# Kernel tuning notes

Hardware: AMD Instinct MI355X
Metric: run time of the kernel (lower is better)

Reference implementation:

```python
import jax, jax.numpy as jnp
import numpy as np

E = 160000      # num edges
N = 10000       # num nodes
M1 = 16         # rep1.mult
M2 = 8          # rep2.mult (output)
D1 = 3          # rep1.dim
D2 = 3          # rep2.dim
NREPS = 2       # repr.nreps()
EDGE_DIM = 32
HID = 64
NHEADS = 4
HIDDEN_SIZE = M2 * D2            # 24, attention hidden size
HEAD_DIM = HIDDEN_SIZE // NHEADS # 6
M2H = 3 * M2                     # repr_h.rep2.mult = 24 (k,q,v fused)
TMP_OUT = NREPS * M1 * M2H       # 768, RadialWeight layer2 out dim


def setup_inputs() -> dict:
    key = jax.random.key(0)
    ks = jax.random.split(key, 9)
    src = jax.random.randint(ks[0], (E,), 0, N)
    dst = jax.random.randint(ks[1], (E,), 0, N)
    basis = jax.random.normal(ks[2], (E, D1, NREPS * D2), dtype=jnp.float32)
    edge_feats = jax.random.normal(ks[3], (E, EDGE_DIM), dtype=jnp.float32)
    f = jax.random.normal(ks[4], (N, M1, D1), dtype=jnp.float32)
    W1 = jax.random.normal(ks[5], (HID, EDGE_DIM), dtype=jnp.float32) * 0.05
    b1 = jnp.zeros((HID,), dtype=jnp.float32)
    W2 = jax.random.normal(ks[6], (TMP_OUT, HID), dtype=jnp.float32) * 0.05
    b2 = jnp.zeros((TMP_OUT,), dtype=jnp.float32)
    return {"src": src, "dst": dst, "basis": basis, "edge_feats": edge_feats,
            "f": f, "W1": W1, "b1": b1, "W2": W2, "b2": b2}


def reference(src, dst, basis, edge_feats, f, W1, b1, W2, b2):
    # --- RadialWeight: 2-layer MLP on invariant edge feats ---
    h = jax.nn.relu(edge_feats @ W1.T + b1)               # (E, HID)
    rw = (h @ W2.T + b2).reshape(E, M2H, M1 * NREPS)      # (E, 3*m2, m1*nreps)

    # --- Equivariant convolution: gather by src, basis matmul, radial mix ---
    fe = f[src]                                           # (E, m1, d1)
    tmp = jnp.einsum('emd,edk->emk', fe, basis)           # (E, m1, nreps*d2)
    tmp = tmp.reshape(E, M1 * NREPS, D2)                  # (E, m1*nreps, d2)
    conv = jnp.einsum('ecm,emd->ecd', rw, tmp)            # (E, 3*m2, d2)

    # --- split into k, q, v along the multiplicity (feature) dim ---
    k, q, v = jnp.split(conv, 3, axis=1)                  # each (E, m2, d2)
    k = k.reshape(E, NHEADS, HEAD_DIM)
    q = q.reshape(E, NHEADS, HEAD_DIM)
    v = v.reshape(E, NHEADS, HEAD_DIM)

    # --- graph attention: LeakyReLU scores + edge softmax over dst ---
    temp = HIDDEN_SIZE ** (-0.5)
    scores = jnp.sum(k * q, axis=-1) * temp               # (E, NHEADS)
    scores = jax.nn.leaky_relu(scores, negative_slope=0.2)
    smax = jax.ops.segment_max(scores, dst, num_segments=N)   # (N, NHEADS)
    ex = jnp.exp(scores - smax[dst])                      # (E, NHEADS)
    denom = jax.ops.segment_sum(ex, dst, num_segments=N)  # (N, NHEADS)
    weights = ex / denom[dst]                             # (E, NHEADS)

    # --- weighted values, scatter-sum to dst nodes ---
    wv = weights[..., None] * v                           # (E, NHEADS, HEAD_DIM)
    out = jax.ops.segment_sum(wv, dst, num_segments=N)    # (N, NHEADS, HEAD_DIM)
    return out.reshape(N, M2, D2)
```

## Files before the change

### kernel.cpp

```cpp
#include <hip/hip_runtime.h>

#define E_EDGES 160000
#define N_NODES 10000
#define SLOTS   64

#define TEMP 0.20412414523193154f

typedef __fp16 half2_t __attribute__((ext_vector_type(2)));
typedef __fp16 half8_t __attribute__((ext_vector_type(8)));
typedef float f32x4 __attribute__((ext_vector_type(4)));

__device__ __forceinline__ float fdot2(half2_t a, half2_t b, float c) {
#if __has_builtin(__builtin_amdgcn_fdot2)
    return __builtin_amdgcn_fdot2(a, b, c, false);
#else
    return fmaf((float)a.x, (float)b.x, fmaf((float)a.y, (float)b.y, c));
#endif
}
__device__ __forceinline__ half2_t pk(float a, float b) {
    return __builtin_amdgcn_cvt_pkrtz(a, b);
}

__global__ __launch_bounds__(256)
void prep_kernel(const float* __restrict__ W2, unsigned* __restrict__ w2p,
                 int* __restrict__ cnt)
{
    int u = blockIdx.x * blockDim.x + threadIdx.x;
    if (u < N_NODES) cnt[u] = 0;
    int tp    = u & 3;
    int lane  = (u >> 2) & 63;
    int piece = (u >> 8) & 3;
    int c     = u >> 10;
    int em = lane & 15, quad = lane >> 4;
    int row = 32*c + ((piece >> 1) << 4) + em;
    int col = ((piece & 1) << 5) + quad*8 + 2*tp;
    union { half2_t h; unsigned v; } o;
    o.h.x = (__fp16)W2[row*64 + col];
    o.h.y = (__fp16)W2[row*64 + col + 1];
    w2p[u] = o.v;
}

#define CONV_GROUP(cbase, OUT) \
    _Pragma("unroll") \
    for (int cg = 0; cg < 8; ++cg) { \
        const int c = (cbase) + cg; \
        const __fp16* base = w2s + ((cg*4)*64 + lane)*8; \
        half8_t wa0 = *(const half8_t*)(base); \
        half8_t wa1 = *(const half8_t*)(base + 64*8); \
        half8_t wb0 = *(const half8_t*)(base + 2*64*8); \
        half8_t wb1 = *(const half8_t*)(base + 3*64*8); \
        float4 bb0 = *(const float4*)(b2s + 32*c + quad*4); \
        float4 bb1 = *(const float4*)(b2s + 32*c + 16 + quad*4); \
        f32x4 acc0 = {bb0.x, bb0.y, bb0.z, bb0.w}; \
        acc0 = __builtin_amdgcn_mfma_f32_16x16x32_f16(wa0, h_lo, acc0, 0, 0, 0); \
        acc0 = __builtin_amdgcn_mfma_f32_16x16x32_f16(wa1, h_hi, acc0, 0, 0, 0); \
        f32x4 acc1 = {bb1.x, bb1.y, bb1.z, bb1.w}; \
        acc1 = __builtin_amdgcn_mfma_f32_16x16x32_f16(wb0, h_lo, acc1, 0, 0, 0); \
        acc1 = __builtin_amdgcn_mfma_f32_16x16x32_f16(wb1, h_hi, acc1, 0, 0, 0); \
        float p0 = 0.f, p1 = 0.f, p2 = 0.f; \
        _Pragma("unroll") \
        for (int r = 0; r < 4; ++r) { \
            half2_t rp = pk(acc0[r], acc1[r]); \
            p0 = fdot2(rp, t2[r][0], p0); \
            p1 = fdot2(rp, t2[r][1], p1); \
            p2 = fdot2(rp, t2[r][2], p2); \
        } \
        p0 += __shfl_xor(p0, 16); p0 += __shfl_xor(p0, 32); \
        p1 += __shfl_xor(p1, 16); p1 += __shfl_xor(p1, 32); \
        p2 += __shfl_xor(p2, 16); p2 += __shfl_xor(p2, 32); \
        OUT; \
    }

#define STAGE_W2(group) { \
    uint4* d4 = (uint4*)w2s; \
    _Pragma("unroll") \
    for (int i = 0; i < 8; ++i) d4[i*256 + tid] = w2p[(group)*2048 + i*256 + tid]; \
}

__global__ __launch_bounds__(256, 3)
void fused_kernel(const int* __restrict__ src, const int* __restrict__ dst,
                  const float* __restrict__ basis, const float* __restrict__ efeat,
                  const float* __restrict__ f,
                  const float* __restrict__ W1, const float* __restrict__ b1,
                  const uint4* __restrict__ w2p, const float* __restrict__ b2,
                  float* __restrict__ v_out, float* __restrict__ sc_out,
                  int* __restrict__ cnt, int* __restrict__ idx)
{
    __shared__ __fp16 w2s[8*4*64*8];
    __shared__ float  w1s[64*32];
    __shared__ float  b2s[768];

    const int tid  = threadIdx.x;
    const int lane = tid & 63;
    const int wid  = tid >> 6;
    const int em   = lane & 15;
    const int quad = lane >> 4;
    const int e = (blockIdx.x * 4 + wid) * 16 + em;

    STAGE_W2(0);
    {
        float4* w14 = (float4*)w1s;
        const float4* W14 = (const float4*)W1;
        w14[tid] = W14[tid];
        w14[256 + tid] = W14[256 + tid];
        if (tid < 192) ((float4*)b2s)[tid] = ((const float4*)b2)[tid];
    }

    if (quad == 0) {
        int dn = dst[e];
        int p = atomicAdd(&cnt[dn], 1);
        if (p < SLOTS) idx[dn*SLOTS + p] = e;
    }

    __syncthreads();

    half8_t h_lo, h_hi;
    {
        float x[32];
        const float4* xv = (const float4*)(efeat + (size_t)e * 32);
        #pragma unroll
        for (int i = 0; i < 8; ++i) {
            float4 t = xv[i];
            x[4*i+0] = t.x; x[4*i+1] = t.y; x[4*i+2] = t.z; x[4*i+3] = t.w;
        }
        union { __fp16 h[8]; half8_t v; } lo, hi;
        #pragma unroll
        for (int t = 0; t < 8; ++t) {
            const int j0 = quad*8 + t;
            const int j1 = 32 + quad*8 + t;
            float a0 = b1[j0], a1 = b1[j1];
            const float* __restrict__ w0 = w1s + j0*32;
            const float* __restrict__ w1 = w1s + j1*32;
            #pragma unroll
            for (int i = 0; i < 32; ++i) {
                a0 = fmaf(w0[i], x[i], a0);
                a1 = fmaf(w1[i], x[i], a1);
            }
            lo.h[t] = (__fp16)fmaxf(a0, 0.0f);
            hi.h[t] = (__fp16)fmaxf(a1, 0.0f);
        }
        h_lo = lo.v; h_hi = hi.v;
    }

    half2_t t2[4][3];
    {
        float bas[18];
        const float2* bv = (const float2*)(basis + (size_t)e * 18);
        #pragma unroll
        for (int i = 0; i < 9; ++i) { float2 t = bv[i]; bas[2*i] = t.x; bas[2*i+1] = t.y; }
        const float* fp = f + (size_t)src[e] * 48 + quad*6;
        float fl[6], fh[6];
        #pragma unroll
        for (int i = 0; i < 3; ++i) {
            float2 a = *(const float2*)(fp + 2*i);      fl[2*i] = a.x; fl[2*i+1] = a.y;
            float2 b = *(const float2*)(fp + 24 + 2*i); fh[2*i] = b.x; fh[2*i+1] = b.y;
        }
        #pragma unroll
        for (int jj = 0; jj < 4; ++jj) {
            const int mr = (jj >> 1) * 3;
            const int rb = (jj & 1) * 3;
            #pragma unroll
            for (int d = 0; d < 3; ++d) {
                float lo = fmaf(fl[mr+0], bas[rb+d],
                           fmaf(fl[mr+1], bas[6+rb+d], fl[mr+2] * bas[12+rb+d]));
                float hi = fmaf(fh[mr+0], bas[rb+d],
                           fmaf(fh[mr+1], bas[6+rb+d], fh[mr+2] * bas[12+rb+d]));
                t2[jj][d] = pk(lo, hi);
            }
        }
    }

    float kreg[8][3];
    CONV_GROUP(0, { kreg[cg][0]=p0; kreg[cg][1]=p1; kreg[cg][2]=p2; });

    __syncthreads();
    STAGE_W2(1);
    __syncthreads();
    float sreg[4];
    CONV_GROUP(8, {
        float s_ = p0*kreg[cg][0] + p1*kreg[cg][1] + p2*kreg[cg][2];
        if ((cg & 1) == 0) sreg[cg>>1] = s_; else sreg[cg>>1] += s_;
    });

    #pragma unroll
    for (int hh = 0; hh < 4; ++hh) {
        float s = sreg[hh] * TEMP;
        sreg[hh] = (s > 0.0f) ? s : 0.2f * s;
    }
    if (quad == 3) {
        *(float4*)(sc_out + (size_t)e*4) = make_float4(sreg[0], sreg[1], sreg[2], sreg[3]);
    }

    __syncthreads();
    STAGE_W2(2);
    __syncthreads();
    float vreg[8][3];
    CONV_GROUP(16, { vreg[cg][0]=p0; vreg[cg][1]=p1; vreg[cg][2]=p2; });

    float* vb = v_out + (size_t)e * 24;
    if (quad == 0) {
        *(float4*)(vb+0) = make_float4(vreg[0][0], vreg[0][1], vreg[0][2], vreg[1][0]);
        *(float4*)(vb+4) = make_float4(vreg[1][1], vreg[1][2], vreg[2][0], vreg[2][1]);
    } else if (quad == 1) {
        *(float4*)(vb+8)  = make_float4(vreg[2][2], vreg[3][0], vreg[3][1], vreg[3][2]);
        *(float4*)(vb+12) = make_float4(vreg[4][0], vreg[4][1], vreg[4][2], vreg[5][0]);
    } else if (quad == 2) {
        *(float4*)(vb+16) = make_float4(vreg[5][1], vreg[5][2], vreg[6][0], vreg[6][1]);
        *(float4*)(vb+20) = make_float4(vreg[6][2], vreg[7][0], vreg[7][1], vreg[7][2]);
    }
}

__global__ __launch_bounds__(256)
void gather_kernel(const int* __restrict__ cnt, const int* __restrict__ idx,
                   const float* __restrict__ sc, const float* __restrict__ v,
                   float* __restrict__ out)
{
    const int lane = threadIdx.x & 63;
    const int wid  = threadIdx.x >> 6;
    const int n = blockIdx.x * 4 + wid;
    if (n >= N_NODES) return;
    int deg = cnt[n];
    if (deg > SLOTS) deg = SLOTS;
    const int* __restrict__ nb = idx + n * SLOTS;

    const int i2 = lane >> 2, h = lane & 3;
    float m = -1e30f;
    for (int i = i2; i < deg; i += 16) {
        m = fmaxf(m, sc[nb[i]*4 + h]);
    }
    m = fmaxf(m, __shfl_xor(m, 4));
    m = fmaxf(m, __shfl_xor(m, 8));
    m = fmaxf(m, __shfl_xor(m, 16));
    m = fmaxf(m, __shfl_xor(m, 32));

    const int j = lane & 31;
    const int half = lane >> 5;
    const int hd = (j < 24) ? (j / 6) : 0;
    float mh = __shfl(m, hd);

    float acc = 0.f, den = 0.f;
    if (j < 24) {
        for (int i = half; i < deg; i += 2) {
            int eid = nb[i];
            float ex = __expf(sc[eid*4 + hd] - mh);
            den += ex;
            acc = fmaf(ex, v[eid*24 + j], acc);
        }
    }
    acc += __shfl_xor(acc, 32);
    den += __shfl_xor(den, 32);
    if (half == 0 && j < 24) {
        out[n*24 + j] = (den > 0.f) ? (acc / den) : 0.f;
    }
}

extern "C" void kernel_launch(void* const* d_in, const int* in_sizes, int n_in,
                              void* d_out, int out_size, void* d_ws, size_t ws_size,
                              hipStream_t stream)
{
    const int*   src   = (const int*)d_in[0];
    const int*   dst   = (const int*)d_in[1];
    const float* basis = (const float*)d_in[2];
    const float* ef    = (const float*)d_in[3];
    const float* f     = (const float*)d_in[4];
    const float* W1    = (const float*)d_in[5];
    const float* b1    = (const float*)d_in[6];
    const float* W2    = (const float*)d_in[7];
    const float* b2    = (const float*)d_in[8];
    float* out = (float*)d_out;

    float*    v_buf  = (float*)d_ws;
    float*    sc_buf = v_buf + (size_t)E_EDGES * 24;
    unsigned* w2p    = (unsigned*)(sc_buf + (size_t)E_EDGES * 4);
    int*      cnt    = (int*)(w2p + 24576);
    int*      idx    = cnt + N_NODES;

    prep_kernel<<<96, 256, 0, stream>>>(W2, w2p, cnt);

    fused_kernel<<<E_EDGES / 64, 256, 0, stream>>>(src, dst, basis, ef, f,
                                                   W1, b1, (const uint4*)w2p, b2,
                                                   v_buf, sc_buf, cnt, idx);

    gather_kernel<<<(N_NODES + 3) / 4, 256, 0, stream>>>(cnt, idx, sc_buf, v_buf, out);
}
```

Measured before the change: 165.4 us.

## Replace bucketed softmax gather with atomic scatter of unnormalized exp-weighted values

```diff
diff --git a/kernel.cpp b/kernel.cpp
--- a/kernel.cpp
+++ b/kernel.cpp
@@ -2,7 +2,6 @@
 
 #define E_EDGES 160000
 #define N_NODES 10000
-#define SLOTS   64
 
 #define TEMP 0.20412414523193154f
 
@@ -21,12 +20,20 @@
     return __builtin_amdgcn_cvt_pkrtz(a, b);
 }
 
+__device__ __forceinline__ int w1swz(int u) {
+    return (u & ~7) | ((u & 7) ^ ((u >> 6) & 3));
+}
+
 __global__ __launch_bounds__(256)
 void prep_kernel(const float* __restrict__ W2, unsigned* __restrict__ w2p,
-                 int* __restrict__ cnt)
+                 float4* __restrict__ zbuf)
 {
     int u = blockIdx.x * blockDim.x + threadIdx.x;
-    if (u < N_NODES) cnt[u] = 0;
+    #pragma unroll
+    for (int i = 0; i < 3; ++i) {
+        int z = u + i * 24576;
+        if (z < (N_NODES * 28) / 4) zbuf[z] = make_float4(0.f, 0.f, 0.f, 0.f);
+    }
     int tp    = u & 3;
     int lane  = (u >> 2) & 63;
     int piece = (u >> 8) & 3;
@@ -83,8 +90,7 @@
                   const float* __restrict__ f,
                   const float* __restrict__ W1, const float* __restrict__ b1,
                   const uint4* __restrict__ w2p, const float* __restrict__ b2,
-                  float* __restrict__ v_out, float* __restrict__ sc_out,
-                  int* __restrict__ cnt, int* __restrict__ idx)
+                  float* __restrict__ num, float* __restrict__ den)
 {
     __shared__ __fp16 w2s[8*4*64*8];
     __shared__ float  w1s[64*32];
@@ -96,20 +102,15 @@
     const int em   = lane & 15;
     const int quad = lane >> 4;
     const int e = (blockIdx.x * 4 + wid) * 16 + em;
+    const int dn = dst[e];
 
     STAGE_W2(0);
     {
         float4* w14 = (float4*)w1s;
         const float4* W14 = (const float4*)W1;
-        w14[tid] = W14[tid];
-        w14[256 + tid] = W14[256 + tid];
+        w14[w1swz(tid)]       = W14[tid];
+        w14[w1swz(256 + tid)] = W14[256 + tid];
         if (tid < 192) ((float4*)b2s)[tid] = ((const float4*)b2)[tid];
-    }
-
-    if (quad == 0) {
-        int dn = dst[e];
-        int p = atomicAdd(&cnt[dn], 1);
-        if (p < SLOTS) idx[dn*SLOTS + p] = e;
     }
 
     __syncthreads();
@@ -129,12 +130,21 @@
             const int j0 = quad*8 + t;
             const int j1 = 32 + quad*8 + t;
             float a0 = b1[j0], a1 = b1[j1];
-            const float* __restrict__ w0 = w1s + j0*32;
-            const float* __restrict__ w1 = w1s + j1*32;
+            const float4* r0 = (const float4*)w1s + j0*8;
+            const float4* r1 = (const float4*)w1s + j1*8;
             #pragma unroll
-            for (int i = 0; i < 32; ++i) {
-                a0 = fmaf(w0[i], x[i], a0);
-                a1 = fmaf(w1[i], x[i], a1);
+            for (int l = 0; l < 8; ++l) {
+                const int ip = l ^ quad;
+                float4 wa = r0[ip];
+                float4 wb = r1[ip];
+                a0 = fmaf(wa.x, x[4*l+0], a0);
+                a0 = fmaf(wa.y, x[4*l+1], a0);
+                a0 = fmaf(wa.z, x[4*l+2], a0);
+                a0 = fmaf(wa.w, x[4*l+3], a0);
+                a1 = fmaf(wb.x, x[4*l+0], a1);
+                a1 = fmaf(wb.y, x[4*l+1], a1);
+                a1 = fmaf(wb.z, x[4*l+2], a1);
+                a1 = fmaf(wb.w, x[4*l+3], a1);
             }
             lo.h[t] = (__fp16)fmaxf(a0, 0.0f);
             hi.h[t] = (__fp16)fmaxf(a1, 0.0f);
@@ -182,13 +192,12 @@
         if ((cg & 1) == 0) sreg[cg>>1] = s_; else sreg[cg>>1] += s_;
     });
 
+    float exv[4];
     #pragma unroll
     for (int hh = 0; hh < 4; ++hh) {
         float s = sreg[hh] * TEMP;
-        sreg[hh] = (s > 0.0f) ? s : 0.2f * s;
-    }
-    if (quad == 3) {
-        *(float4*)(sc_out + (size_t)e*4) = make_float4(sreg[0], sreg[1], sreg[2], sreg[3]);
+        s = (s > 0.0f) ? s : 0.2f * s;
+        exv[hh] = __expf(s);
     }
 
     __syncthreads();
@@ -197,61 +206,54 @@
     float vreg[8][3];
     CONV_GROUP(16, { vreg[cg][0]=p0; vreg[cg][1]=p1; vreg[cg][2]=p2; });
 
-    float* vb = v_out + (size_t)e * 24;
+    float* nb = num + (size_t)dn * 24;
     if (quad == 0) {
-        *(float4*)(vb+0) = make_float4(vreg[0][0], vreg[0][1], vreg[0][2], vreg[1][0]);
-        *(float4*)(vb+4) = make_float4(vreg[1][1], vreg[1][2], vreg[2][0], vreg[2][1]);
+        atomicAdd(nb+0, exv[0]*vreg[0][0]);
+        atomicAdd(nb+1, exv[0]*vreg[0][1]);
+        atomicAdd(nb+2, exv[0]*vreg[0][2]);
+        atomicAdd(nb+3, exv[0]*vreg[1][0]);
+        atomicAdd(nb+4, exv[0]*vreg[1][1]);
+        atomicAdd(nb+5, exv[0]*vreg[1][2]);
+        atomicAdd(nb+6, exv[1]*vreg[2][0]);
+        atomicAdd(nb+7, exv[1]*vreg[2][1]);
     } else if (quad == 1) {
-        *(float4*)(vb+8)  = make_float4(vreg[2][2], vreg[3][0], vreg[3][1], vreg[3][2]);
-        *(float4*)(vb+12) = make_float4(vreg[4][0], vreg[4][1], vreg[4][2], vreg[5][0]);
+        atomicAdd(nb+8,  exv[1]*vreg[2][2]);
+        atomicAdd(nb+9,  exv[1]*vreg[3][0]);
+        atomicAdd(nb+10, exv[1]*vreg[3][1]);
+        atomicAdd(nb+11, exv[1]*vreg[3][2]);
+        atomicAdd(nb+12, exv[2]*vreg[4][0]);
+        atomicAdd(nb+13, exv[2]*vreg[4][1]);
+        atomicAdd(nb+14, exv[2]*vreg[4][2]);
+        atomicAdd(nb+15, exv[2]*vreg[5][0]);
     } else if (quad == 2) {
-        *(float4*)(vb+16) = make_float4(vreg[5][1], vreg[5][2], vreg[6][0], vreg[6][1]);
-        *(float4*)(vb+20) = make_float4(vreg[6][2], vreg[7][0], vreg[7][1], vreg[7][2]);
+        atomicAdd(nb+16, exv[2]*vreg[5][1]);
+        atomicAdd(nb+17, exv[2]*vreg[5][2]);
+        atomicAdd(nb+18, exv[3]*vreg[6][0]);
+        atomicAdd(nb+19, exv[3]*vreg[6][1]);
+        atomicAdd(nb+20, exv[3]*vreg[6][2]);
+        atomicAdd(nb+21, exv[3]*vreg[7][0]);
+        atomicAdd(nb+22, exv[3]*vreg[7][1]);
+        atomicAdd(nb+23, exv[3]*vreg[7][2]);
+    } else {
+        float* db = den + (size_t)dn * 4;
+        atomicAdd(db+0, exv[0]);
+        atomicAdd(db+1, exv[1]);
+        atomicAdd(db+2, exv[2]);
+        atomicAdd(db+3, exv[3]);
     }
 }
 
 __global__ __launch_bounds__(256)
-void gather_kernel(const int* __restrict__ cnt, const int* __restrict__ idx,
-                   const float* __restrict__ sc, const float* __restrict__ v,
-                   float* __restrict__ out)
-{
-    const int lane = threadIdx.x & 63;
-    const int wid  = threadIdx.x >> 6;
-    const int n = blockIdx.x * 4 + wid;
-    if (n >= N_NODES) return;
-    int deg = cnt[n];
-    if (deg > SLOTS) deg = SLOTS;
-    const int* __restrict__ nb = idx + n * SLOTS;
-
-    const int i2 = lane >> 2, h = lane & 3;
-    float m = -1e30f;
-    for (int i = i2; i < deg; i += 16) {
-        m = fmaxf(m, sc[nb[i]*4 + h]);
-    }
-    m = fmaxf(m, __shfl_xor(m, 4));
-    m = fmaxf(m, __shfl_xor(m, 8));
-    m = fmaxf(m, __shfl_xor(m, 16));
-    m = fmaxf(m, __shfl_xor(m, 32));
-
-    const int j = lane & 31;
-    const int half = lane >> 5;
-    const int hd = (j < 24) ? (j / 6) : 0;
-    float mh = __shfl(m, hd);
-
-    float acc = 0.f, den = 0.f;
-    if (j < 24) {
-        for (int i = half; i < deg; i += 2) {
-            int eid = nb[i];
-            float ex = __expf(sc[eid*4 + hd] - mh);
-            den += ex;
-            acc = fmaf(ex, v[eid*24 + j], acc);
-        }
-    }
-    acc += __shfl_xor(acc, 32);
-    den += __shfl_xor(den, 32);
-    if (half == 0 && j < 24) {
-        out[n*24 + j] = (den > 0.f) ? (acc / den) : 0.f;
-    }
+void finalize_kernel(const float* __restrict__ num, const float* __restrict__ den,
+                     float* __restrict__ out)
+{
+    int t = blockIdx.x * 256 + threadIdx.x;
+    if (t >= N_NODES * 24) return;
+    int n = t / 24;
+    int j = t - n * 24;
+    int h = j / 6;
+    float d = den[n*4 + h];
+    out[t] = (d > 0.f) ? num[t] / d : 0.f;
 }
 
 extern "C" void kernel_launch(void* const* d_in, const int* in_sizes, int n_in,
@@ -269,17 +271,15 @@
     const float* b2    = (const float*)d_in[8];
     float* out = (float*)d_out;
 
-    float*    v_buf  = (float*)d_ws;
-    float*    sc_buf = v_buf + (size_t)E_EDGES * 24;
-    unsigned* w2p    = (unsigned*)(sc_buf + (size_t)E_EDGES * 4);
-    int*      cnt    = (int*)(w2p + 24576);
-    int*      idx    = cnt + N_NODES;
-
-    prep_kernel<<<96, 256, 0, stream>>>(W2, w2p, cnt);
+    float*    num = (float*)d_ws;
+    float*    den = num + (size_t)N_NODES * 24;
+    unsigned* w2p = (unsigned*)(den + (size_t)N_NODES * 4);
+
+    prep_kernel<<<96, 256, 0, stream>>>(W2, w2p, (float4*)num);
 
     fused_kernel<<<E_EDGES / 64, 256, 0, stream>>>(src, dst, basis, ef, f,
                                                    W1, b1, (const uint4*)w2p, b2,
-                                                   v_buf, sc_buf, cnt, idx);
-
-    gather_kernel<<<(N_NODES + 3) / 4, 256, 0, stream>>>(cnt, idx, sc_buf, v_buf, out);
-}
+                                                   num, den);
+
+    finalize_kernel<<<(N_NODES * 24 + 255) / 256, 256, 0, stream>>>(num, den, out);
+}
```

New measurement: 343.4 us. +107.6%, slower.
